# Kernel optimization log

Hardware: AMD Instinct MI355X
Metric: run time of the kernel (lower is better)

## Reference

```python
import jax, jax.numpy as jnp
import numpy as np

N_NODES = 50000
N_EDGES = 800000
NNIN = 128
NOPEN = 64
NLAYER = 8
NUM_OUT = 40
H = 0.1  # integration step h


def setup_inputs() -> dict:
    key = jax.random.key(0)
    k1, k2, k3, k4, k5, k6 = jax.random.split(key, 6)
    xn = jax.random.normal(k1, (1, NNIN, N_NODES), dtype=jnp.float32)
    I = jax.random.randint(k2, (N_EDGES,), 0, N_NODES)
    J = jax.random.randint(k3, (N_EDGES,), 0, N_NODES)
    K1Nopen = jax.random.normal(k4, (NOPEN, NNIN), dtype=jnp.float32) * 0.01
    # identityInit: square per-layer kernels near identity
    eye = jnp.eye(NOPEN, dtype=jnp.float32)
    KN2 = eye[None, :, :] + jax.random.normal(k5, (NLAYER, NOPEN, NOPEN), dtype=jnp.float32) * 0.01
    KNclose = jax.random.normal(k6, (NUM_OUT, NOPEN), dtype=jnp.float32) * 0.01
    return {"xn": xn, "I": I, "J": J, "n_nodes": N_NODES,
            "K1Nopen": K1Nopen, "KN2": KN2, "KNclose": KNclose}


def gcn_norm(I, J, n_nodes):
    # PyG gcn_norm with self-loops: w = D^-1/2 A_hat D^-1/2 (deg over col index)
    loop = jnp.arange(n_nodes)
    I2 = jnp.concatenate([I, loop])
    J2 = jnp.concatenate([J, loop])
    w = jnp.ones(I2.shape[0], dtype=jnp.float32)
    deg = jax.ops.segment_sum(w, J2, num_segments=n_nodes)
    dinv = jnp.where(deg > 0, 1.0 / jnp.sqrt(deg), 0.0)
    W = dinv[I2] * w * dinv[J2]
    return I2, J2, W


def reference(xn, I, J, n_nodes, K1Nopen, KN2, KNclose):
    I2, J2, W = gcn_norm(I, J, n_nodes)
    We = W[None, None, :]  # broadcast over [batch, channel, edge]

    # opening 1x1 conv + relu (K1Nopen non-square branch of singleLayer)
    xn = jax.nn.relu(jnp.einsum('oc,bcn->bon', K1Nopen, xn))
    xn_old = xn

    def step(carry, K):
        xn, xn_old = carry
        # nodeGrad: gather + weighted difference -> [1, C, E]
        g = We * (xn[:, :, I2] - xn[:, :, J2])
        # square singleLayer (relu=False): conv(K) -> tanh -> conv(K.T)
        t = jnp.tanh(jnp.einsum('oc,bce->boe', K, g))
        d = jnp.einsum('co,boe->bce', K, t)
        # edgeDiv: weighted scatter-add back to nodes
        dW = We * d
        dxn = jnp.zeros_like(xn).at[:, :, I2].add(dW).at[:, :, J2].add(-dW)
        # leapfrog wave integration
        xn_new = 2.0 * xn - xn_old - (H * H) * dxn
        return (xn_new, xn), None

    (xn, xn_old), _ = jax.lax.scan(step, (xn, xn_old), KN2)

    # closing 1x1 conv, then squeeze().t() -> [n_nodes, num_output]
    out = jnp.einsum('oc,bcn->bon', KNclose, xn)
    return out[0].T
```

## Files before the change

### kernel.cpp

```cpp
#include <hip/hip_runtime.h>
#include <hip/hip_bf16.h>
#include <hip/hip_fp16.h>

#define N_NODES 50000
#define N_EDGES 800000
#define NNIN    128
#define NOPEN   64
#define NUM_OUT 40
#define NLAYER  8
#define HSQ     0.01f

#define NDIG  ((N_NODES + 255) >> 8)
#define EPB   2048
#define P1B   ((N_EDGES + EPB - 1) / EPB)
#define P2CAP 9216
#define SBIN  32
#define ENT_CAP 3200000

typedef float f32x2 __attribute__((ext_vector_type(2)));
typedef int   i32x4 __attribute__((ext_vector_type(4)));
typedef int   i32x2 __attribute__((ext_vector_type(2)));

__device__ __forceinline__ f32x2 pk_fma(f32x2 a, f32x2 b, f32x2 c) {
    f32x2 d;
    asm("v_pk_fma_f32 %0, %1, %2, %3" : "=v"(d) : "v"(a), "v"(b), "v"(c));
    return d;
}

__device__ __forceinline__ void gload4(i32x4 &d, unsigned vo, const void* b) {
    asm volatile("global_load_dwordx4 %0, %1, %2" : "=v"(d) : "v"(vo), "s"(b));
}
__device__ __forceinline__ void gload2(i32x2 &d, unsigned vo, const void* b) {
    asm volatile("global_load_dwordx2 %0, %1, %2" : "=v"(d) : "v"(vo), "s"(b));
}
__device__ __forceinline__ void gload1(unsigned &d, unsigned vo, const void* b) {
    asm volatile("global_load_dword %0, %1, %2" : "=v"(d) : "v"(vo), "s"(b));
}
#define WAITCNT(n) do { asm volatile("s_waitcnt vmcnt(" #n ")"); \
                        __builtin_amdgcn_sched_barrier(0); } while (0)


__global__ void deg_init(int* __restrict__ degi) {
    int n = blockIdx.x * 256 + threadIdx.x;
    if (n < N_NODES) degi[n] = 1;
}

__global__ __launch_bounds__(256) void count_all(const int* __restrict__ I,
                                                 const int* __restrict__ J,
                                                 int* __restrict__ degi,
                                                 int* __restrict__ bh) {
    __shared__ int h[NDIG];
    int t = threadIdx.x, b = blockIdx.x;
    for (int i = t; i < NDIG; i += 256) h[i] = 0;
    __syncthreads();
    int e0 = b * EPB;
    int e1 = min(e0 + EPB, N_EDGES);
    for (int e = e0 + t; e < e1; e += 256) {
        int i = I[e], j = J[e];
        atomicAdd(&degi[j], 1);
        atomicAdd(&h[i >> 8], 1);
        atomicAdd(&h[j >> 8], 1);
    }
    __syncthreads();
    for (int i = t; i < NDIG; i += 256) bh[b * NDIG + i] = h[i];
}

__global__ void calc_dinv(const int* __restrict__ degi, float* __restrict__ dinv) {
    int n = blockIdx.x * 256 + threadIdx.x;
    if (n < N_NODES) dinv[n] = rsqrtf((float)degi[n]);
}

__global__ __launch_bounds__(512) void col_scan(const int* __restrict__ bh,
                                                int* __restrict__ off,
                                                int* __restrict__ total) {
    __shared__ int sh[512];
    int d = blockIdx.x, t = threadIdx.x;
    int v = (t < P1B) ? bh[t * NDIG + d] : 0;
    sh[t] = v;
    __syncthreads();
#pragma unroll
    for (int o = 1; o < 512; o <<= 1) {
        int x = (t >= o) ? sh[t - o] : 0;
        __syncthreads();
        sh[t] += x;
        __syncthreads();
    }
    if (t < P1B) off[d * P1B + t] = sh[t] - v;
    if (t == 511) total[d] = sh[511];
}

__global__ __launch_bounds__(256) void dig_scan(const int* __restrict__ total,
                                                int* __restrict__ dig_raw,
                                                int* __restrict__ dig_pad) {
    __shared__ int sh[256], sh2[256];
    int t = threadIdx.x;
    int v   = (t < NDIG) ? total[t] : 0;
    int cap = (t < NDIG) ? ((v + 256 * 31 + 7) & ~7) : 0;
    sh[t] = v; sh2[t] = cap;
    __syncthreads();
#pragma unroll
    for (int o = 1; o < 256; o <<= 1) {
        int x = (t >= o) ? sh[t - o] : 0;
        int y = (t >= o) ? sh2[t - o] : 0;
        __syncthreads();
        sh[t] += x; sh2[t] += y;
        __syncthreads();
    }
    if (t < NDIG) { dig_raw[t] = sh[t] - v; dig_pad[t] = sh2[t] - cap; }
}

__global__ __launch_bounds__(256) void pass1_scatter(const int* __restrict__ I,
                                                     const int* __restrict__ J,
                                                     const int* __restrict__ off,
                                                     const int* __restrict__ dig_raw,
                                                     unsigned* __restrict__ ebuf) {
    __shared__ int cnt2[NDIG];
    __shared__ int base[NDIG];
    int t = threadIdx.x, b = blockIdx.x;
    for (int i = t; i < NDIG; i += 256) {
        cnt2[i] = 0;
        base[i] = dig_raw[i] + off[i * P1B + b];
    }
    __syncthreads();
    int e0 = b * EPB;
    int e1 = min(e0 + EPB, N_EDGES);
    for (int e = e0 + t; e < e1; e += 256) {
        int i = I[e], j = J[e];
        int li = atomicAdd(&cnt2[i >> 8], 1);
        ebuf[base[i >> 8] + li] = ((unsigned)i << 16) | (unsigned)j;
        int lj = atomicAdd(&cnt2[j >> 8], 1);
        ebuf[base[j >> 8] + lj] = ((unsigned)j << 16) | (unsigned)i;
    }
}

__global__ __launch_bounds__(256) void pass2_csr(const unsigned* __restrict__ ebuf,
                                                 const int* __restrict__ dig_raw,
                                                 const int* __restrict__ total,
                                                 const int* __restrict__ dig_pad,
                                                 const float* __restrict__ dinv,
                                                 int* __restrict__ row_start,
                                                 int* __restrict__ deg2,
                                                 unsigned short* __restrict__ eid,
                                                 unsigned* __restrict__ ewt) {
    __shared__ unsigned eb[P2CAP];
    __shared__ int cnt[256], loc[256], cur[256];
    int d = blockIdx.x, t = threadIdx.x;
    int s = dig_raw[d];
    int c = total[d]; if (c > P2CAP) c = P2CAP;
    for (int i = t; i < c; i += 256) eb[i] = ebuf[s + i];
    cnt[t] = 0;
    __syncthreads();
    for (int i = t; i < c; i += 256)
        atomicAdd(&cnt[(eb[i] >> 16) & 255], 1);
    __syncthreads();
    int ch = (cnt[t] + 7) >> 3;
    ch = (ch + 3) & ~3;
    int pc = ch << 3;
    loc[t] = pc;
    __syncthreads();
#pragma unroll
    for (int o = 1; o < 256; o <<= 1) {
        int x = (t >= o) ? loc[t - o] : 0;
        __syncthreads();
        loc[t] += x;
        __syncthreads();
    }
    int mybase = dig_pad[d] + loc[t] - pc;
    int n = (d << 8) + t;
    if (n < N_NODES) {
        row_start[n] = mybase;
        deg2[n] = cnt[t];
    }
    cur[t] = mybase;
    __syncthreads();
    for (int i = t; i < c; i += 256) {
        unsigned v = eb[i];
        int ln = (int)(v >> 16) & 255;
        int other = (int)(v & 0xffffu);
        int p = atomicAdd(&cur[ln], 1);
        float w = dinv[(d << 8) + ln] * dinv[other];
        eid[p] = (unsigned short)other;
        ewt[p] = __builtin_bit_cast(unsigned, __float2half2_rn(w));
    }
    __syncthreads();
    if (n < N_NODES) {
        for (int p = mybase + cnt[t]; p < mybase + pc; p++) {
            eid[p] = (unsigned short)n;
            ewt[p] = 0u;
        }
    }
}

__global__ __launch_bounds__(256) void sort_hist(const int* __restrict__ deg2,
                                                 int* __restrict__ sbh) {
    __shared__ int h[SBIN];
    int t = threadIdx.x, b = blockIdx.x;
    if (t < SBIN) h[t] = 0;
    __syncthreads();
    int n = b * 256 + t;
    if (n < N_NODES) atomicAdd(&h[min(deg2[n], 255) >> 3], 1);
    __syncthreads();
    if (t < SBIN) sbh[b * SBIN + t] = h[t];
}

__global__ __launch_bounds__(256) void sort_scan(const int* __restrict__ sbh,
                                                 int* __restrict__ soff,
                                                 int* __restrict__ stot) {
    __shared__ int sh[256];
    int bin = blockIdx.x, t = threadIdx.x;
    int v = (t < NDIG) ? sbh[t * SBIN + bin] : 0;
    sh[t] = v;
    __syncthreads();
#pragma unroll
    for (int o = 1; o < 256; o <<= 1) {
        int x = (t >= o) ? sh[t - o] : 0;
        __syncthreads();
        sh[t] += x;
        __syncthreads();
    }
    if (t < NDIG) soff[bin * NDIG + t] = sh[t] - v;
    if (t == 255) stot[bin] = sh[255];
}

__global__ void sort_base(const int* __restrict__ stot, int* __restrict__ sbase) {
    int t = threadIdx.x;
    if (t < SBIN) {
        int acc = 0;
        for (int b2 = t + 1; b2 < SBIN; b2++) acc += stot[b2];
        sbase[t] = acc;
    }
}

__global__ __launch_bounds__(256) void sort_scatter(const int* __restrict__ deg2,
                                                    const int* __restrict__ soff,
                                                    const int* __restrict__ sbase,
                                                    int* __restrict__ perm) {
    __shared__ int c[SBIN];
    __shared__ int bb[SBIN];
    int t = threadIdx.x, b = blockIdx.x;
    if (t < SBIN) { c[t] = 0; bb[t] = sbase[t] + soff[t * NDIG + b]; }
    __syncthreads();
    int n = b * 256 + t;
    if (n < N_NODES) {
        int bin = min(deg2[n], 255) >> 3;
        int p = atomicAdd(&c[bin], 1);
        perm[bb[bin] + p] = n;
    }
}

__global__ __launch_bounds__(256) void first_layer(const float* __restrict__ xn,
                                                   const float* __restrict__ k1f,
                                                   float* __restrict__ x_cur,
                                                   float* __restrict__ x_old) {
    __shared__ float Ks[NOPEN * 129];
    __shared__ float xs[32 * 64];
    int t = threadIdx.x;
    int n0 = blockIdx.x * 64;
    for (int idx = t; idx < NOPEN * NNIN; idx += 256)
        Ks[(idx >> 7) * 129 + (idx & 127)] = k1f[idx];

    int tn = t & 15, to = t >> 4;
    float acc[4][4] = {};
    for (int c0 = 0; c0 < NNIN; c0 += 32) {
        __syncthreads();
        for (int idx = t; idx < 32 * 64; idx += 256) {
            int ci = idx >> 6, n = idx & 63;
            int gn = n0 + n;
            xs[ci * 64 + n] = (gn < N_NODES) ? xn[(size_t)(c0 + ci) * N_NODES + gn] : 0.f;
        }
        __syncthreads();
        for (int ci = 0; ci < 32; ci++) {
            float xv[4], kv[4];
#pragma unroll
            for (int i2 = 0; i2 < 4; i2++) xv[i2] = xs[ci * 64 + tn * 4 + i2];
#pragma unroll
            for (int j = 0; j < 4; j++) kv[j] = Ks[(to * 4 + j) * 129 + c0 + ci];
#pragma unroll
            for (int i2 = 0; i2 < 4; i2++)
#pragma unroll
                for (int j = 0; j < 4; j++) acc[i2][j] += xv[i2] * kv[j];
        }
    }
#pragma unroll
    for (int i2 = 0; i2 < 4; i2++) {
        int node = n0 + tn * 4 + i2;
        if (node < N_NODES) {
            float4 st;
            st.x = fmaxf(acc[i2][0], 0.f);
            st.y = fmaxf(acc[i2][1], 0.f);
            st.z = fmaxf(acc[i2][2], 0.f);
            st.w = fmaxf(acc[i2][3], 0.f);
            *(float4*)&x_cur[(size_t)node * 64 + to * 4] = st;
            *(float4*)&x_old[(size_t)node * 64 + to * 4] = st;
        }
    }
}

__global__ __launch_bounds__(256) void mat_y(const float* __restrict__ x,
                                             const float* __restrict__ K,
                                             __half* __restrict__ Y) {
    __shared__ float Ks[64 * 65];
    __shared__ float xs[64 * 65];
    int t = threadIdx.x, n0 = blockIdx.x * 64;
    for (int idx = t; idx < 4096; idx += 256) {
        int r = idx >> 6, c = idx & 63;
        Ks[r * 65 + c] = K[idx];
        int gn = n0 + r;
        xs[r * 65 + c] = (gn < N_NODES) ? x[(size_t)gn * 64 + c] : 0.f;
    }
    __syncthreads();
    int tn = t & 15, to = t >> 4;
    float acc[4][4] = {};
    for (int c = 0; c < 64; c++) {
        float xv[4], kv[4];
#pragma unroll
        for (int i2 = 0; i2 < 4; i2++) xv[i2] = xs[(tn * 4 + i2) * 65 + c];
#pragma unroll
        for (int j = 0; j < 4; j++) kv[j] = Ks[(to * 4 + j) * 65 + c];
#pragma unroll
        for (int i2 = 0; i2 < 4; i2++)
#pragma unroll
            for (int j = 0; j < 4; j++) acc[i2][j] += xv[i2] * kv[j];
    }
#pragma unroll
    for (int i2 = 0; i2 < 4; i2++) {
        int node = n0 + tn * 4 + i2;
        if (node < N_NODES) {
            __half2 h0 = __floats2half2_rn(acc[i2][0], acc[i2][1]);
            __half2 h1 = __floats2half2_rn(acc[i2][2], acc[i2][3]);
            __half2* dst = (__half2*)&Y[(size_t)node * 64 + to * 4];
            dst[0] = h0;
            dst[1] = h1;
        }
    }
}

__global__ __launch_bounds__(512, 6) void gather_update(
        const __half* __restrict__ Y,
        const float* __restrict__ x_cur,
        const float* __restrict__ x_old,
        const unsigned short* __restrict__ eid,
        const unsigned* __restrict__ ewt,
        const int* __restrict__ row_start,
        const int* __restrict__ deg2,
        const int* __restrict__ perm,
        const float* __restrict__ K,
        const float* __restrict__ Kn,
        float* __restrict__ x_out,
        __half* __restrict__ Y_out) {
    __shared__ float Ks[64 * 66];
    __shared__ float Ksn[64 * 66];
    __shared__ float Ss[8][64];
    int t = threadIdx.x;
    int wv = t >> 6, lane = t & 63;
    int c2  = lane & 31;
    int sel = lane >> 5;
    int n = __builtin_amdgcn_readfirstlane(perm[blockIdx.x * 8 + wv]);

    int beg = row_start[n];
    int dg  = deg2[n];
    __half2 yn16 = *(const __half2*)&Y[((size_t)n << 6) + 2 * c2];
    float xc = x_cur[(size_t)n * 64 + lane];
    float xo = x_old[(size_t)n * 64 + lane];

    for (int idx = t; idx < 4096; idx += 512) {
        int r = idx >> 6, cc = idx & 63;
        Ks[r * 66 + cc]  = K[idx];
        Ksn[r * 66 + cc] = Kn[idx];
    }
    __syncthreads();

    beg = __builtin_amdgcn_readfirstlane(beg);
    dg  = __builtin_amdgcn_readfirstlane(dg);
    int ch = (dg + 7) >> 3;
    int nch4 = (ch + 3) & ~3;

    const __half2 C3h  = __float2half2_rn(-0.33333334f);
    const __half2 C5h  = __float2half2_rn( 0.13333334f);
    const __half2 C7h  = __float2half2_rn(-0.053968254f);
    const __half2 ONEh = __float2half2_rn( 1.0f);
    __half2 s16 = __float2half2_rn(0.f);

#define EDGE_ACC(gu, wu)                                                     \
    {                                                                        \
        __half2 gh = __builtin_bit_cast(__half2, (unsigned)(gu));            \
        __half2 wh = __builtin_bit_cast(__half2, (unsigned)(wu));            \
        __half2 dd = __hsub2(yn16, gh);                                      \
        __half2 zz = __hmul2(wh, dd);                                        \
        __half2 z2 = __hmul2(zz, zz);                                        \
        __half2 pp = __hfma2(z2, __hfma2(z2, __hfma2(z2, C7h, C5h), C3h), ONEh); \
        __half2 u  = __hmul2(wh, zz);                                        \
        s16 = __hfma2(u, pp, s16);                                           \
    }

    if (nch4 > 0) {
        int lastc = nch4 - 1;
        int begi = beg * 2;
        int begw = beg * 4;
        unsigned seli = (unsigned)(sel << 3);
        unsigned selw = (unsigned)(sel << 4);
        unsigned c2b  = (unsigned)(c2 << 2);
        const void* eidv = (const void*)eid;
        const void* ewtv = (const void*)ewt;
        const void* Yv   = (const void*)Y;

        i32x2 Id0, Id1, Id2, Id3;
        i32x4 W0, W1, W2, W3;
        unsigned G00, G01, G02, G03, G10, G11, G12, G13;
        unsigned G20, G21, G22, G23, G30, G31, G32, G33;

        gload2(Id0, (unsigned)(begi)       + seli, eidv);
        gload4(W0,  (unsigned)(begw)       + selw, ewtv);
        gload2(Id1, (unsigned)(begi + 16)  + seli, eidv);
        gload4(W1,  (unsigned)(begw + 32)  + selw, ewtv);
        gload2(Id2, (unsigned)(begi + 32)  + seli, eidv);
        gload4(W2,  (unsigned)(begw + 64)  + selw, ewtv);
        WAITCNT(4);
        {
            unsigned u0 = (unsigned)Id0.x, u1 = (unsigned)Id0.y;
            gload1(G00, ((u0 & 0xffffu) << 7) + c2b, Yv);
            gload1(G01, ((u0 >> 16)     << 7) + c2b, Yv);
            gload1(G02, ((u1 & 0xffffu) << 7) + c2b, Yv);
            gload1(G03, ((u1 >> 16)     << 7) + c2b, Yv);
        }
        gload2(Id3, (unsigned)(begi + 48)  + seli, eidv);
        gload4(W3,  (unsigned)(begw + 96)  + selw, ewtv);
        WAITCNT(8);
        {
            unsigned u0 = (unsigned)Id1.x, u1 = (unsigned)Id1.y;
            gload1(G10, ((u0 & 0xffffu) << 7) + c2b, Yv);
            gload1(G11, ((u0 >> 16)     << 7) + c2b, Yv);
            gload1(G12, ((u1 & 0xffffu) << 7) + c2b, Yv);
            gload1(G13, ((u1 >> 16)     << 7) + c2b, Yv);
        }

#define STAGE(sa, sb)                                                        \
        {                                                                    \
            WAITCNT(6);                       \
            EDGE_ACC(G##sa##0, W##sa.x)                                      \
            EDGE_ACC(G##sa##1, W##sa.y)                                      \
            EDGE_ACC(G##sa##2, W##sa.z)                                      \
            EDGE_ACC(G##sa##3, W##sa.w)                                      \
            {                                                                \
                int kc = min(c + 4, lastc);                                  \
                gload2(Id##sa, (unsigned)(begi + kc * 16) + seli, eidv);     \
                gload4(W##sa,  (unsigned)(begw + kc * 32) + selw, ewtv);     \
                unsigned u0 = (unsigned)Id##sb.x, u1 = (unsigned)Id##sb.y;   \
                gload1(G##sb##0, ((u0 & 0xffffu) << 7) + c2b, Yv);           \
                gload1(G##sb##1, ((u0 >> 16)     << 7) + c2b, Yv);           \
                gload1(G##sb##2, ((u1 & 0xffffu) << 7) + c2b, Yv);           \
                gload1(G##sb##3, ((u1 >> 16)     << 7) + c2b, Yv);           \
            }                                                                \
            c++;                                                             \
        }

        int c = 0;
        while (c < nch4) {
            STAGE(0, 2)
            STAGE(1, 3)
            STAGE(2, 0)
            STAGE(3, 1)
        }
#undef STAGE
        asm volatile("s_waitcnt vmcnt(0)");
        __builtin_amdgcn_sched_barrier(0);
    }
#undef EDGE_ACC

    float2 sf = __half22float2(s16);
    float sx = sf.x, sy = sf.y;
    sx += __shfl_xor(sx, 32, 64);
    sy += __shfl_xor(sy, 32, 64);
    if (lane < 32) {
        Ss[wv][2 * c2]     = sx;
        Ss[wv][2 * c2 + 1] = sy;
    }
    f32x2 acc2 = {0.f, 0.f};
#pragma unroll
    for (int o = 0; o < 64; o += 2)
        acc2 = pk_fma(*(const f32x2*)&Ks[lane * 66 + o],
                      *(const f32x2*)&Ss[wv][o], acc2);
    float xnew = 2.f * xc - xo - HSQ * (acc2.x + acc2.y);
    __builtin_nontemporal_store(xnew, &x_out[(size_t)n * 64 + lane]);
    Ss[wv][lane] = xnew;
    f32x2 acc3 = {0.f, 0.f};
#pragma unroll
    for (int cc = 0; cc < 64; cc += 2)
        acc3 = pk_fma(*(const f32x2*)&Ksn[lane * 66 + cc],
                      *(const f32x2*)&Ss[wv][cc], acc3);
    Y_out[((size_t)n << 6) + lane] = __float2half(acc3.x + acc3.y);
}

__global__ __launch_bounds__(256) void out_kernel(const float* __restrict__ x,
                                                  const float* __restrict__ Kc,
                                                  float* __restrict__ out) {
    __shared__ float xs[64 * 65];
    __shared__ float Ks[40 * 65];
    int t = threadIdx.x, n0 = blockIdx.x * 64;
    for (int idx = t; idx < 4096; idx += 256) {
        int r = idx >> 6, c = idx & 63;
        int gn = n0 + r;
        xs[r * 65 + c] = (gn < N_NODES) ? x[(size_t)gn * 64 + c] : 0.f;
    }
    for (int idx = t; idx < NUM_OUT * 64; idx += 256) {
        int r = idx >> 6, c = idx & 63;
        Ks[r * 65 + c] = Kc[idx];
    }
    __syncthreads();
    if (t < 160) {
        int tn = t & 15, to = t >> 4;
        float acc[4][4] = {};
        for (int c = 0; c < 64; c++) {
            float xv[4], kv[4];
#pragma unroll
            for (int i2 = 0; i2 < 4; i2++) xv[i2] = xs[(tn * 4 + i2) * 65 + c];
#pragma unroll
            for (int j = 0; j < 4; j++) kv[j] = Ks[(to * 4 + j) * 65 + c];
#pragma unroll
            for (int i2 = 0; i2 < 4; i2++)
#pragma unroll
                for (int j = 0; j < 4; j++) acc[i2][j] += xv[i2] * kv[j];
        }
#pragma unroll
        for (int i2 = 0; i2 < 4; i2++) {
            int node = n0 + tn * 4 + i2;
            if (node < N_NODES) {
#pragma unroll
                for (int j = 0; j < 4; j++)
                    out[(size_t)node * NUM_OUT + to * 4 + j] = acc[i2][j];
            }
        }
    }
}

extern "C" void kernel_launch(void* const* d_in, const int* in_sizes, int n_in,
                              void* d_out, int out_size, void* d_ws, size_t ws_size,
                              hipStream_t stream) {
    const float* xn = (const float*)d_in[0];
    const int*   I  = (const int*)d_in[1];
    const int*   J  = (const int*)d_in[2];
    const float* K1 = (const float*)d_in[4];
    const float* K2 = (const float*)d_in[5];
    const float* Kc = (const float*)d_in[6];

    const size_t NC = (size_t)N_NODES * NOPEN;
    float*    f       = (float*)d_ws;
    float*    x_cur   = f;
    float*    x_old   = f + NC;
    __half*   Y0      = (__half*)(f + 2 * NC);
    __half*   Y1      = (__half*)(f + 2 * NC + NC / 2);
    float*    dinv    = f + 3 * NC;
    int*      degi    = (int*)(dinv + N_NODES);
    int*      deg2    = degi + N_NODES;
    int*      row_st  = deg2 + N_NODES;
    int*      total   = row_st + N_NODES;
    int*      dig_raw = total + 256;
    int*      dig_pad = dig_raw + 256;
    int*      perm    = dig_pad + 256;
    int*      sbh     = perm + 50048;
    int*      soff    = sbh + 6400;
    int*      stot    = soff + 6400;
    int*      sbase   = stot + 64;
    int*      bh      = sbase + 64;
    int*      off     = bh + 80000;
    unsigned* ewt     = (unsigned*)(off + 80000);
    unsigned short* eid = (unsigned short*)(ewt + ENT_CAP);
    unsigned* ebuf    = (unsigned*)x_cur;

    dim3 B(256);
    const int GN = (N_NODES + 255) / 256;

    deg_init<<<GN, B, 0, stream>>>(degi);
    count_all<<<P1B, B, 0, stream>>>(I, J, degi, bh);
    calc_dinv<<<GN, B, 0, stream>>>(degi, dinv);
    col_scan<<<NDIG, dim3(512), 0, stream>>>(bh, off, total);
    dig_scan<<<1, B, 0, stream>>>(total, dig_raw, dig_pad);
    pass1_scatter<<<P1B, B, 0, stream>>>(I, J, off, dig_raw, ebuf);
    pass2_csr<<<NDIG, B, 0, stream>>>(ebuf, dig_raw, total, dig_pad, dinv,
                                      row_st, deg2, eid, ewt);

    sort_hist<<<NDIG, B, 0, stream>>>(deg2, sbh);
    sort_scan<<<SBIN, B, 0, stream>>>(sbh, soff, stot);
    sort_base<<<1, dim3(64), 0, stream>>>(stot, sbase);
    sort_scatter<<<NDIG, B, 0, stream>>>(deg2, soff, sbase, perm);

    const int NB = (N_NODES + 63) / 64;
    first_layer<<<NB, B, 0, stream>>>(xn, K1, x_cur, x_old);
    mat_y<<<NB, B, 0, stream>>>(x_cur, K2, Y0);

    __half* Yin = Y0;
    __half* Yout = Y1;
    float* xc = x_cur;
    float* xo = x_old;
    for (int l = 0; l < NLAYER; l++) {
        const float* Kl = K2 + l * NOPEN * NOPEN;
        const float* Knext = K2 + (l + 1 < NLAYER ? l + 1 : l) * NOPEN * NOPEN;
        gather_update<<<N_NODES / 8, dim3(512), 0, stream>>>(
            Yin, xc, xo, eid, ewt, row_st, deg2, perm, Kl, Knext, xo, Yout);
        float* tmp = xc; xc = xo; xo = tmp;
        __half* th = Yin; Yin = Yout; Yout = th;
    }
    out_kernel<<<NB, B, 0, stream>>>(xc, Kc, (float*)d_out);
}
```

Before: 727.7 us.

## Pack edge id and fp16 weight into one word; process two nodes per wave

Merges the separate 16-bit neighbour-id and half2 weight arrays into a single 32-bit entry (weight in the high half, id in the low half), so each edge needs one load instead of two streams. Each wave now handles two nodes, one per half-wave, with a deeper 8-stage prefetch pipeline of dwordx4 entry loads, and the grid size is halved. Row padding changes to multiples of 32 with extra slack, and the entry buffer capacity is raised to match. The aim is to cut index/weight load traffic and per-wave overhead. The cost is imbalance when the two paired nodes have different degrees, since the loop runs to the larger count, plus higher register pressure.

```diff
diff --git a/kernel.cpp b/kernel.cpp
--- a/kernel.cpp
+++ b/kernel.cpp
@@ -15,11 +15,10 @@
 #define P1B   ((N_EDGES + EPB - 1) / EPB)
 #define P2CAP 9216
 #define SBIN  32
-#define ENT_CAP 3200000
+#define ENT_CAP 3500000
 
 typedef float f32x2 __attribute__((ext_vector_type(2)));
 typedef int   i32x4 __attribute__((ext_vector_type(4)));
-typedef int   i32x2 __attribute__((ext_vector_type(2)));
 
 __device__ __forceinline__ f32x2 pk_fma(f32x2 a, f32x2 b, f32x2 c) {
     f32x2 d;
@@ -29,9 +28,6 @@
 
 __device__ __forceinline__ void gload4(i32x4 &d, unsigned vo, const void* b) {
     asm volatile("global_load_dwordx4 %0, %1, %2" : "=v"(d) : "v"(vo), "s"(b));
-}
-__device__ __forceinline__ void gload2(i32x2 &d, unsigned vo, const void* b) {
-    asm volatile("global_load_dwordx2 %0, %1, %2" : "=v"(d) : "v"(vo), "s"(b));
 }
 __device__ __forceinline__ void gload1(unsigned &d, unsigned vo, const void* b) {
     asm volatile("global_load_dword %0, %1, %2" : "=v"(d) : "v"(vo), "s"(b));
@@ -95,7 +91,7 @@
     __shared__ int sh[256], sh2[256];
     int t = threadIdx.x;
     int v   = (t < NDIG) ? total[t] : 0;
-    int cap = (t < NDIG) ? ((v + 256 * 31 + 7) & ~7) : 0;
+    int cap = (t < NDIG) ? ((v + 256 * 35 + 31) & ~31) : 0;
     sh[t] = v; sh2[t] = cap;
     __syncthreads();
 #pragma unroll
@@ -140,8 +136,7 @@
                                                  const float* __restrict__ dinv,
                                                  int* __restrict__ row_start,
                                                  int* __restrict__ deg2,
-                                                 unsigned short* __restrict__ eid,
-                                                 unsigned* __restrict__ ewt) {
+                                                 unsigned* __restrict__ ent) {
     __shared__ unsigned eb[P2CAP];
     __shared__ int cnt[256], loc[256], cur[256];
     int d = blockIdx.x, t = threadIdx.x;
@@ -153,9 +148,7 @@
     for (int i = t; i < c; i += 256)
         atomicAdd(&cnt[(eb[i] >> 16) & 255], 1);
     __syncthreads();
-    int ch = (cnt[t] + 7) >> 3;
-    ch = (ch + 3) & ~3;
-    int pc = ch << 3;
+    int pc = (cnt[t] + 35) & ~31;
     loc[t] = pc;
     __syncthreads();
 #pragma unroll
@@ -179,15 +172,13 @@
         int other = (int)(v & 0xffffu);
         int p = atomicAdd(&cur[ln], 1);
         float w = dinv[(d << 8) + ln] * dinv[other];
-        eid[p] = (unsigned short)other;
-        ewt[p] = __builtin_bit_cast(unsigned, __float2half2_rn(w));
+        unsigned w16 = (unsigned)__half_as_ushort(__float2half_rn(w));
+        ent[p] = (w16 << 16) | (unsigned)other;
     }
     __syncthreads();
     if (n < N_NODES) {
-        for (int p = mybase + cnt[t]; p < mybase + pc; p++) {
-            eid[p] = (unsigned short)n;
-            ewt[p] = 0u;
-        }
+        for (int p = mybase + cnt[t]; p < mybase + pc; p++)
+            ent[p] = (unsigned)n;
     }
 }
 
@@ -339,8 +330,7 @@
         const __half* __restrict__ Y,
         const float* __restrict__ x_cur,
         const float* __restrict__ x_old,
-        const unsigned short* __restrict__ eid,
-        const unsigned* __restrict__ ewt,
+        const unsigned* __restrict__ ent,
         const int* __restrict__ row_start,
         const int* __restrict__ deg2,
         const int* __restrict__ perm,
@@ -350,18 +340,20 @@
         __half* __restrict__ Y_out) {
     __shared__ float Ks[64 * 66];
     __shared__ float Ksn[64 * 66];
-    __shared__ float Ss[8][64];
+    __shared__ float Ss[16][64];
     int t = threadIdx.x;
     int wv = t >> 6, lane = t & 63;
     int c2  = lane & 31;
     int sel = lane >> 5;
-    int n = __builtin_amdgcn_readfirstlane(perm[blockIdx.x * 8 + wv]);
-
-    int beg = row_start[n];
-    int dg  = deg2[n];
-    __half2 yn16 = *(const __half2*)&Y[((size_t)n << 6) + 2 * c2];
-    float xc = x_cur[(size_t)n * 64 + lane];
-    float xo = x_old[(size_t)n * 64 + lane];
+    int pbase = blockIdx.x * 16 + (wv << 1);
+    int nA = __builtin_amdgcn_readfirstlane(perm[pbase]);
+    int nB = __builtin_amdgcn_readfirstlane(perm[pbase + 1]);
+    int n_lane = sel ? nB : nA;
+
+    int beg = row_start[n_lane];
+    int dg  = deg2[n_lane];
+    __half2 yn16 = *(const __half2*)&Y[((size_t)n_lane << 6) + 2 * c2];
+    asm volatile("" :: "v"(yn16));
 
     for (int idx = t; idx < 4096; idx += 512) {
         int r = idx >> 6, cc = idx & 63;
@@ -370,10 +362,15 @@
     }
     __syncthreads();
 
-    beg = __builtin_amdgcn_readfirstlane(beg);
-    dg  = __builtin_amdgcn_readfirstlane(dg);
-    int ch = (dg + 7) >> 3;
-    int nch4 = (ch + 3) & ~3;
+    int nch = ((dg + 35) & ~31) >> 2;
+    int nmax = max(nch, __shfl_xor(nch, 32, 64));
+    nmax = __builtin_amdgcn_readfirstlane(nmax);
+
+    unsigned o_base = (unsigned)beg * 4u;
+    unsigned o_last = o_base + (unsigned)(nch - 1) * 16u;
+    unsigned c2b    = (unsigned)(c2 << 2);
+    const void* entv = (const void*)ent;
+    const void* Yv   = (const void*)Y;
 
     const __half2 C3h  = __float2half2_rn(-0.33333334f);
     const __half2 C5h  = __float2half2_rn( 0.13333334f);
@@ -381,10 +378,22 @@
     const __half2 ONEh = __float2half2_rn( 1.0f);
     __half2 s16 = __float2half2_rn(0.f);
 
-#define EDGE_ACC(gu, wu)                                                     \
+    i32x4 E0, E1, E2, E3, E4, E5, E6, E7;
+    unsigned G00, G01, G02, G03, G10, G11, G12, G13;
+    unsigned G20, G21, G22, G23, G30, G31, G32, G33;
+
+#define GATH(Ga, Gb, Gc, Gd, Eg)                                             \
+    {                                                                        \
+        gload1(Ga, (((unsigned)(Eg).x & 0xffffu) << 7) + c2b, Yv);           \
+        gload1(Gb, (((unsigned)(Eg).y & 0xffffu) << 7) + c2b, Yv);           \
+        gload1(Gc, (((unsigned)(Eg).z & 0xffffu) << 7) + c2b, Yv);           \
+        gload1(Gd, (((unsigned)(Eg).w & 0xffffu) << 7) + c2b, Yv);           \
+    }
+#define EDGE_ACC(gu, eu)                                                     \
     {                                                                        \
         __half2 gh = __builtin_bit_cast(__half2, (unsigned)(gu));            \
-        __half2 wh = __builtin_bit_cast(__half2, (unsigned)(wu));            \
+        __half2 wh = __half2half2(__high2half(                               \
+                         __builtin_bit_cast(__half2, (unsigned)(eu))));      \
         __half2 dd = __hsub2(yn16, gh);                                      \
         __half2 zz = __hmul2(wh, dd);                                        \
         __half2 z2 = __hmul2(zz, zz);                                        \
@@ -393,102 +402,84 @@
         s16 = __hfma2(u, pp, s16);                                           \
     }
 
-    if (nch4 > 0) {
-        int lastc = nch4 - 1;
-        int begi = beg * 2;
-        int begw = beg * 4;
-        unsigned seli = (unsigned)(sel << 3);
-        unsigned selw = (unsigned)(sel << 4);
-        unsigned c2b  = (unsigned)(c2 << 2);
-        const void* eidv = (const void*)eid;
-        const void* ewtv = (const void*)ewt;
-        const void* Yv   = (const void*)Y;
-
-        i32x2 Id0, Id1, Id2, Id3;
-        i32x4 W0, W1, W2, W3;
-        unsigned G00, G01, G02, G03, G10, G11, G12, G13;
-        unsigned G20, G21, G22, G23, G30, G31, G32, G33;
-
-        gload2(Id0, (unsigned)(begi)       + seli, eidv);
-        gload4(W0,  (unsigned)(begw)       + selw, ewtv);
-        gload2(Id1, (unsigned)(begi + 16)  + seli, eidv);
-        gload4(W1,  (unsigned)(begw + 32)  + selw, ewtv);
-        gload2(Id2, (unsigned)(begi + 32)  + seli, eidv);
-        gload4(W2,  (unsigned)(begw + 64)  + selw, ewtv);
-        WAITCNT(4);
-        {
-            unsigned u0 = (unsigned)Id0.x, u1 = (unsigned)Id0.y;
-            gload1(G00, ((u0 & 0xffffu) << 7) + c2b, Yv);
-            gload1(G01, ((u0 >> 16)     << 7) + c2b, Yv);
-            gload1(G02, ((u1 & 0xffffu) << 7) + c2b, Yv);
-            gload1(G03, ((u1 >> 16)     << 7) + c2b, Yv);
-        }
-        gload2(Id3, (unsigned)(begi + 48)  + seli, eidv);
-        gload4(W3,  (unsigned)(begw + 96)  + selw, ewtv);
-        WAITCNT(8);
-        {
-            unsigned u0 = (unsigned)Id1.x, u1 = (unsigned)Id1.y;
-            gload1(G10, ((u0 & 0xffffu) << 7) + c2b, Yv);
-            gload1(G11, ((u0 >> 16)     << 7) + c2b, Yv);
-            gload1(G12, ((u1 & 0xffffu) << 7) + c2b, Yv);
-            gload1(G13, ((u1 >> 16)     << 7) + c2b, Yv);
-        }
-
-#define STAGE(sa, sb)                                                        \
-        {                                                                    \
-            WAITCNT(6);                       \
-            EDGE_ACC(G##sa##0, W##sa.x)                                      \
-            EDGE_ACC(G##sa##1, W##sa.y)                                      \
-            EDGE_ACC(G##sa##2, W##sa.z)                                      \
-            EDGE_ACC(G##sa##3, W##sa.w)                                      \
-            {                                                                \
-                int kc = min(c + 4, lastc);                                  \
-                gload2(Id##sa, (unsigned)(begi + kc * 16) + seli, eidv);     \
-                gload4(W##sa,  (unsigned)(begw + kc * 32) + selw, ewtv);     \
-                unsigned u0 = (unsigned)Id##sb.x, u1 = (unsigned)Id##sb.y;   \
-                gload1(G##sb##0, ((u0 & 0xffffu) << 7) + c2b, Yv);           \
-                gload1(G##sb##1, ((u0 >> 16)     << 7) + c2b, Yv);           \
-                gload1(G##sb##2, ((u1 & 0xffffu) << 7) + c2b, Yv);           \
-                gload1(G##sb##3, ((u1 >> 16)     << 7) + c2b, Yv);           \
-            }                                                                \
-            c++;                                                             \
-        }
-
-        int c = 0;
-        while (c < nch4) {
-            STAGE(0, 2)
-            STAGE(1, 3)
-            STAGE(2, 0)
-            STAGE(3, 1)
-        }
+    gload4(E0, o_base,        entv);
+    gload4(E1, o_base + 16u,  entv);
+    gload4(E2, o_base + 32u,  entv);
+    gload4(E3, o_base + 48u,  entv);
+    gload4(E4, o_base + 64u,  entv);
+    WAITCNT(4);
+    GATH(G00, G01, G02, G03, E0)
+    gload4(E5, o_base + 80u,  entv);
+    WAITCNT(8);
+    GATH(G10, G11, G12, G13, E1)
+    gload4(E6, o_base + 96u,  entv);
+    WAITCNT(12);
+    GATH(G20, G21, G22, G23, E2)
+    gload4(E7, o_base + 112u, entv);
+    WAITCNT(16);
+    GATH(G30, G31, G32, G33, E3)
+
+    unsigned o_cur = o_base;
+
+#define STAGE(Eo, Eg, Ga, Gb, Gc, Gd)                                        \
+    {                                                                        \
+        WAITCNT(15);                                                         \
+        EDGE_ACC(Ga, (Eo).x)                                                 \
+        EDGE_ACC(Gb, (Eo).y)                                                 \
+        EDGE_ACC(Gc, (Eo).z)                                                 \
+        EDGE_ACC(Gd, (Eo).w)                                                 \
+        gload4(Eo, min(o_cur + 128u, o_last), entv);                         \
+        GATH(Ga, Gb, Gc, Gd, Eg)                                             \
+        o_cur += 16u;                                                        \
+    }
+
+    int c = 0;
+    while (c < nmax) {
+        STAGE(E0, E4, G00, G01, G02, G03)
+        STAGE(E1, E5, G10, G11, G12, G13)
+        STAGE(E2, E6, G20, G21, G22, G23)
+        STAGE(E3, E7, G30, G31, G32, G33)
+        STAGE(E4, E0, G00, G01, G02, G03)
+        STAGE(E5, E1, G10, G11, G12, G13)
+        STAGE(E6, E2, G20, G21, G22, G23)
+        STAGE(E7, E3, G30, G31, G32, G33)
+        c += 8;
+    }
 #undef STAGE
-        asm volatile("s_waitcnt vmcnt(0)");
-        __builtin_amdgcn_sched_barrier(0);
-    }
+    asm volatile("s_waitcnt vmcnt(0)");
+    __builtin_amdgcn_sched_barrier(0);
 #undef EDGE_ACC
+#undef GATH
 
     float2 sf = __half22float2(s16);
-    float sx = sf.x, sy = sf.y;
-    sx += __shfl_xor(sx, 32, 64);
-    sy += __shfl_xor(sy, 32, 64);
-    if (lane < 32) {
-        Ss[wv][2 * c2]     = sx;
-        Ss[wv][2 * c2 + 1] = sy;
-    }
-    f32x2 acc2 = {0.f, 0.f};
-#pragma unroll
-    for (int o = 0; o < 64; o += 2)
-        acc2 = pk_fma(*(const f32x2*)&Ks[lane * 66 + o],
-                      *(const f32x2*)&Ss[wv][o], acc2);
-    float xnew = 2.f * xc - xo - HSQ * (acc2.x + acc2.y);
-    __builtin_nontemporal_store(xnew, &x_out[(size_t)n * 64 + lane]);
-    Ss[wv][lane] = xnew;
-    f32x2 acc3 = {0.f, 0.f};
-#pragma unroll
-    for (int cc = 0; cc < 64; cc += 2)
-        acc3 = pk_fma(*(const f32x2*)&Ksn[lane * 66 + cc],
-                      *(const f32x2*)&Ss[wv][cc], acc3);
-    Y_out[((size_t)n << 6) + lane] = __float2half(acc3.x + acc3.y);
+    int sr = (wv << 1) + sel;
+    Ss[sr][2 * c2]     = sf.x;
+    Ss[sr][2 * c2 + 1] = sf.y;
+    float xcA = x_cur[(size_t)nA * 64 + lane];
+    float xoA = x_old[(size_t)nA * 64 + lane];
+    float xcB = x_cur[(size_t)nB * 64 + lane];
+    float xoB = x_old[(size_t)nB * 64 + lane];
+    int rA = wv << 1, rB = rA + 1;
+    f32x2 a2 = {0.f, 0.f}, b2 = {0.f, 0.f};
+#pragma unroll
+    for (int o = 0; o < 64; o += 2) {
+        a2 = pk_fma(*(const f32x2*)&Ks[lane * 66 + o], *(const f32x2*)&Ss[rA][o], a2);
+        b2 = pk_fma(*(const f32x2*)&Ks[lane * 66 + o], *(const f32x2*)&Ss[rB][o], b2);
+    }
+    float xnewA = 2.f * xcA - xoA - HSQ * (a2.x + a2.y);
+    float xnewB = 2.f * xcB - xoB - HSQ * (b2.x + b2.y);
+    __builtin_nontemporal_store(xnewA, &x_out[(size_t)nA * 64 + lane]);
+    __builtin_nontemporal_store(xnewB, &x_out[(size_t)nB * 64 + lane]);
+    Ss[rA][lane] = xnewA;
+    Ss[rB][lane] = xnewB;
+    f32x2 a3 = {0.f, 0.f}, b3 = {0.f, 0.f};
+#pragma unroll
+    for (int cc = 0; cc < 64; cc += 2) {
+        a3 = pk_fma(*(const f32x2*)&Ksn[lane * 66 + cc], *(const f32x2*)&Ss[rA][cc], a3);
+        b3 = pk_fma(*(const f32x2*)&Ksn[lane * 66 + cc], *(const f32x2*)&Ss[rB][cc], b3);
+    }
+    Y_out[((size_t)nA << 6) + lane] = __float2half(a3.x + a3.y);
+    Y_out[((size_t)nB << 6) + lane] = __float2half(b3.x + b3.y);
 }
 
 __global__ __launch_bounds__(256) void out_kernel(const float* __restrict__ x,
@@ -563,8 +554,7 @@
     int*      sbase   = stot + 64;
     int*      bh      = sbase + 64;
     int*      off     = bh + 80000;
-    unsigned* ewt     = (unsigned*)(off + 80000);
-    unsigned short* eid = (unsigned short*)(ewt + ENT_CAP);
+    unsigned* ent     = (unsigned*)(off + 80000);
     unsigned* ebuf    = (unsigned*)x_cur;
 
     dim3 B(256);
@@ -577,7 +567,7 @@
     dig_scan<<<1, B, 0, stream>>>(total, dig_raw, dig_pad);
     pass1_scatter<<<P1B, B, 0, stream>>>(I, J, off, dig_raw, ebuf);
     pass2_csr<<<NDIG, B, 0, stream>>>(ebuf, dig_raw, total, dig_pad, dinv,
-                                      row_st, deg2, eid, ewt);
+                                      row_st, deg2, ent);
 
     sort_hist<<<NDIG, B, 0, stream>>>(deg2, sbh);
     sort_scan<<<SBIN, B, 0, stream>>>(sbh, soff, stot);
@@ -595,8 +585,8 @@
     for (int l = 0; l < NLAYER; l++) {
         const float* Kl = K2 + l * NOPEN * NOPEN;
         const float* Knext = K2 + (l + 1 < NLAYER ? l + 1 : l) * NOPEN * NOPEN;
-        gather_update<<<N_NODES / 8, dim3(512), 0, stream>>>(
-            Yin, xc, xo, eid, ewt, row_st, deg2, perm, Kl, Knext, xo, Yout);
+        gather_update<<<N_NODES / 16, dim3(512), 0, stream>>>(
+            Yin, xc, xo, ent, row_st, deg2, perm, Kl, Knext, xo, Yout);
         float* tmp = xc; xc = xo; xo = tmp;
         __half* th = Yin; Yin = Yout; Yout = th;
     }
```

Measured after the change: 651.9 us. -10.4%, faster.
